# Optimization experiments

Measured on AMD Instinct MI355X. Metric: run time of the kernel, lower is better.

## Reference

```python
import math
import jax, jax.numpy as jnp
import numpy as np

B, NH, T, N, D = 4, 8, 2048, 256, 512
THETA = 2 ** 16
LN_EPS = 1e-5
RETRIEVAL_SCALE = 1.0
TWO_PI = 2.0 * math.pi


def _freqs(n):
    # get_freqs: 1/theta**(floor(i/2)*2 / n) / (2*pi)
    i = jnp.arange(n, dtype=jnp.float32)
    q = jnp.floor(i / 2.0) * 2.0
    return 1.0 / (THETA ** (q / n)) / TWO_PI


def _rope(phases, v):
    # phases: [1,1,T,N]; v: [B,nh,T,N]
    ph = (phases % 1.0) * TWO_PI
    pc, ps = jnp.cos(ph), jnp.sin(ph)
    ve, vo = v[..., ::2], v[..., 1::2]
    v_rot = jnp.stack((-vo, ve), axis=-1).reshape(v.shape)  # interleaved rotate
    return v * pc + v_rot * ps


def _l2norm(x):
    return x / jnp.maximum(jnp.linalg.norm(x, axis=-1, keepdims=True), 1e-12)


def setup_inputs() -> dict:
    key = jax.random.key(0)
    ks = jax.random.split(key, 8)
    return {
        "Q": jax.random.normal(ks[0], (B, NH, T, N), jnp.float32),
        "V": jax.random.normal(ks[1], (B, NH, T, D), jnp.float32),
        "x_raw": jax.random.normal(ks[2], (B, T, D), jnp.float32),
        "x_next": jax.random.normal(ks[3], (B, T, D), jnp.float32),
        "theta_Q_w": 0.02 * jax.random.normal(ks[4], (N, D), jnp.float32),
        "theta_K_w": 0.02 * jax.random.normal(ks[5], (N, D), jnp.float32),
        "beta_w": 0.02 * jax.random.normal(ks[6], (NH, D), jnp.float32),
        "memory_gate": jnp.full((1, NH, 1, 1), -2.0, jnp.float32),
        "M0": 0.02 * jax.random.normal(ks[7], (B, NH, N, D), jnp.float32),
    }


def _forward(Q, V, x_raw, x_next, theta_Q_w, theta_K_w, beta_w, memory_gate, M0):
    Bq, nh, Tq, Nq = Q.shape
    # ---- causal RoPE linear attention (K is Q; strictly lower-triangular, no softmax)
    freqs = _freqs(Nq)  # [N]
    phases = jnp.arange(Tq, dtype=jnp.float32)[None, None, :, None] * freqs[None, None, None, :]
    QR = _rope(phases, Q)
    scores = jnp.einsum('bhtn,bhsn->bhts', QR, QR)
    mask = jnp.tril(jnp.ones((Tq, Tq), bool), -1)  # diagonal=-1
    scores = jnp.where(mask, scores, 0.0)
    y_standard = scores @ V  # [B,nh,T,D]

    # ---- memory retrieval (position-invariant query)
    Qm = _l2norm(x_raw @ theta_Q_w.T)  # [B,T,N], shared across heads
    y_memory = jnp.einsum('btn,bhnd->bhtd', Qm, M0)
    mu = y_memory.mean(-1, keepdims=True)
    var = y_memory.var(-1, keepdims=True)  # biased, like torch LayerNorm
    y_memory = (y_memory - mu) * jax.lax.rsqrt(var + LN_EPS) * RETRIEVAL_SCALE

    # ---- delta-rule memory update (detached in the original)
    Km = _l2norm(jax.lax.stop_gradient(x_raw @ theta_K_w.T))         # [B,T,N]
    beta = jax.nn.sigmoid(jax.lax.stop_gradient(x_raw @ beta_w.T))   # [B,T,nh]
    Vm = jax.lax.stop_gradient(x_next)                               # [B,T,D]
    M_init = jax.lax.stop_gradient(M0)

    def step(M, inp):
        k, v, b = inp  # k:[B,N] shared across heads, v:[B,D], b:[B,nh]
        v_old = jnp.einsum('bn,bhnd->bhd', k, M)
        v_new = b[..., None] * v[:, None, :] + (1.0 - b[..., None]) * v_old
        M = M + jnp.einsum('bn,bhd->bhnd', k, v_new - v_old)
        return M, None

    M_new, _ = jax.lax.scan(
        step, M_init,
        (jnp.swapaxes(Km, 0, 1), jnp.swapaxes(Vm, 0, 1), jnp.swapaxes(beta, 0, 1)))

    gate = jax.nn.sigmoid(memory_gate)  # [1,nh,1,1]
    y = (1.0 - gate) * y_standard + gate * y_memory
    return y, M_new


def reference(Q, V, x_raw, x_next, theta_Q_w, theta_K_w, beta_w, memory_gate, M0):
    return _forward(Q, V, x_raw, x_next, theta_Q_w, theta_K_w, beta_w, memory_gate, M0)
```

## Files before the change

### kernel.cpp

```cpp
#include <hip/hip_runtime.h>
#include <hip/hip_bf16.h>
#include <math.h>

#define BBATCH 4
#define NHEAD  8
#define TSEQ   2048
#define NDIM   256
#define DDIM   512

typedef float f32x4 __attribute__((ext_vector_type(4)));
typedef short bf16x8 __attribute__((ext_vector_type(8)));

typedef __attribute__((address_space(3))) unsigned int lds_uint;
typedef __attribute__((address_space(1))) unsigned int g_uint;

__device__ __forceinline__ unsigned short f2bf(float f) {
  __hip_bfloat16 h = __float2bfloat16(f);
  return *reinterpret_cast<unsigned short*>(&h);
}
__device__ __forceinline__ float bf2f(unsigned short u) {
  __hip_bfloat16 h;
  *reinterpret_cast<unsigned short*>(&h) = u;
  return __bfloat162float(h);
}
__device__ __forceinline__ f32x4 mfma16(bf16x8 a, bf16x8 b, f32x4 c) {
  return __builtin_amdgcn_mfma_f32_16x16x32_bf16(a, b, c, 0, 0, 0);
}

#define KSW(t) (((((t) & 7) ^ (((t) >> 3) & 3))) << 4)

__global__ __launch_bounds__(256) void rope_kernel(const float* __restrict__ Q,
                                                   unsigned short* __restrict__ QR) {
  long idx = (long)blockIdx.x * 256 + threadIdx.x;
  int pair = (int)(idx & 127);
  long row = idx >> 7;
  int t = (int)(row & (TSEQ - 1));
  float2 q = reinterpret_cast<const float2*>(Q)[idx];
  float freq = exp2f(-(float)pair * 0.125f) * 0.15915494309189535f;
  float phase = (float)t * freq;
  float ph = (phase - floorf(phase)) * 6.283185307179586f;
  float s, c;
  sincosf(ph, &s, &c);
  float o0 = q.x * c - q.y * s;
  float o1 = q.y * c + q.x * s;
  unsigned int pk = (unsigned int)f2bf(o0) | ((unsigned int)f2bf(o1) << 16);
  reinterpret_cast<unsigned int*>(QR)[idx] = pk;
}

__global__ __launch_bounds__(256) void transpose_cast_kernel(
    const float* __restrict__ in, unsigned short* __restrict__ out, int R, int C) {
  __shared__ float tile[64][65];
  long mat = blockIdx.z;
  const float* src = in + mat * (long)R * C;
  unsigned short* dst = out + mat * (long)R * C;
  int c0 = blockIdx.x * 64, r0 = blockIdx.y * 64;
  int tr = threadIdx.x >> 4;
  int tc = (threadIdx.x & 15) * 4;
#pragma unroll
  for (int p = 0; p < 4; ++p) {
    int r = tr + p * 16;
    float4 v = *reinterpret_cast<const float4*>(&src[(long)(r0 + r) * C + c0 + tc]);
    tile[r][tc + 0] = v.x; tile[r][tc + 1] = v.y;
    tile[r][tc + 2] = v.z; tile[r][tc + 3] = v.w;
  }
  __syncthreads();
#pragma unroll
  for (int p = 0; p < 4; ++p) {
    int c = tr + p * 16;
    ushort4 o;
    o.x = f2bf(tile[tc + 0][c]);
    o.y = f2bf(tile[tc + 1][c]);
    o.z = f2bf(tile[tc + 2][c]);
    o.w = f2bf(tile[tc + 3][c]);
    *reinterpret_cast<ushort4*>(&dst[(long)(c0 + c) * R + r0 + tc]) = o;
  }
}

__global__ __launch_bounds__(512) void qkm_kernel(
    const float* __restrict__ x,
    const float* __restrict__ wq,
    const float* __restrict__ wk,
    unsigned short* __restrict__ Qm,
    float* __restrict__ Km,
    unsigned short* __restrict__ Kmb) {
  const bool isK = (blockIdx.y == 1);
  const float* w = isK ? wk : wq;
  int r0 = blockIdx.x * 64;
  int wave = threadIdx.x >> 6, lane = threadIdx.x & 63;
  int wm = wave >> 2, wn = wave & 3;
  int khi = lane >> 4, l16 = lane & 15;
  __shared__ unsigned short Ahi[64 * 32], Alo[64 * 32];
  __shared__ unsigned short Bhi[256 * 32], Blo[256 * 32];
  __shared__ float red[4][64];
  f32x4 acc[2][4] = {};
  for (int k0 = 0; k0 < 512; k0 += 32) {
    {
      int row = threadIdx.x >> 3;
      int kc = (threadIdx.x & 7) * 4;
      float4 v = *reinterpret_cast<const float4*>(&x[(long)(r0 + row) * 512 + k0 + kc]);
      float vv[4] = {v.x, v.y, v.z, v.w};
      unsigned int hx[2], lx[2];
      unsigned short h0 = f2bf(vv[0]), h1 = f2bf(vv[1]), h2 = f2bf(vv[2]), h3 = f2bf(vv[3]);
      hx[0] = (unsigned)h0 | ((unsigned)h1 << 16);
      hx[1] = (unsigned)h2 | ((unsigned)h3 << 16);
      lx[0] = (unsigned)f2bf(vv[0] - bf2f(h0)) | ((unsigned)f2bf(vv[1] - bf2f(h1)) << 16);
      lx[1] = (unsigned)f2bf(vv[2] - bf2f(h2)) | ((unsigned)f2bf(vv[3] - bf2f(h3)) << 16);
      int byt = row * 64 + ((kc * 2) ^ ((row & 3) << 4));
      *reinterpret_cast<uint2*>((char*)Ahi + byt) = make_uint2(hx[0], hx[1]);
      *reinterpret_cast<uint2*>((char*)Alo + byt) = make_uint2(lx[0], lx[1]);
    }
#pragma unroll
    for (int p = 0; p < 4; ++p) {
      int idx2 = threadIdx.x + p * 512;
      int row = idx2 >> 3;
      int kc = (idx2 & 7) * 4;
      float4 v = *reinterpret_cast<const float4*>(&w[(long)row * 512 + k0 + kc]);
      float vv[4] = {v.x, v.y, v.z, v.w};
      unsigned short h0 = f2bf(vv[0]), h1 = f2bf(vv[1]), h2 = f2bf(vv[2]), h3 = f2bf(vv[3]);
      unsigned int hx0 = (unsigned)h0 | ((unsigned)h1 << 16);
      unsigned int hx1 = (unsigned)h2 | ((unsigned)h3 << 16);
      unsigned int lx0 = (unsigned)f2bf(vv[0] - bf2f(h0)) | ((unsigned)f2bf(vv[1] - bf2f(h1)) << 16);
      unsigned int lx1 = (unsigned)f2bf(vv[2] - bf2f(h2)) | ((unsigned)f2bf(vv[3] - bf2f(h3)) << 16);
      int byt = row * 64 + ((kc * 2) ^ ((row & 3) << 4));
      *reinterpret_cast<uint2*>((char*)Bhi + byt) = make_uint2(hx0, hx1);
      *reinterpret_cast<uint2*>((char*)Blo + byt) = make_uint2(lx0, lx1);
    }
    __syncthreads();
    bf16x8 ah[2], al[2], bh[4], bl[4];
#pragma unroll
    for (int mi = 0; mi < 2; ++mi) {
      int row = wm * 32 + mi * 16 + l16;
      int byt = row * 64 + ((khi * 16) ^ ((row & 3) << 4));
      ah[mi] = *reinterpret_cast<const bf16x8*>((const char*)Ahi + byt);
      al[mi] = *reinterpret_cast<const bf16x8*>((const char*)Alo + byt);
    }
#pragma unroll
    for (int ni = 0; ni < 4; ++ni) {
      int row = wn * 64 + ni * 16 + l16;
      int byt = row * 64 + ((khi * 16) ^ ((row & 3) << 4));
      bh[ni] = *reinterpret_cast<const bf16x8*>((const char*)Bhi + byt);
      bl[ni] = *reinterpret_cast<const bf16x8*>((const char*)Blo + byt);
    }
#pragma unroll
    for (int mi = 0; mi < 2; ++mi)
#pragma unroll
      for (int ni = 0; ni < 4; ++ni) {
        acc[mi][ni] = mfma16(ah[mi], bh[ni], acc[mi][ni]);
        acc[mi][ni] = mfma16(ah[mi], bl[ni], acc[mi][ni]);
        acc[mi][ni] = mfma16(al[mi], bh[ni], acc[mi][ni]);
      }
    __syncthreads();
  }
  float part[2][4];
#pragma unroll
  for (int mi = 0; mi < 2; ++mi)
#pragma unroll
    for (int r = 0; r < 4; ++r) {
      float s = 0.f;
#pragma unroll
      for (int ni = 0; ni < 4; ++ni) s += acc[mi][ni][r] * acc[mi][ni][r];
      part[mi][r] = s;
    }
#pragma unroll
  for (int off = 1; off < 16; off <<= 1)
#pragma unroll
    for (int mi = 0; mi < 2; ++mi)
#pragma unroll
      for (int r = 0; r < 4; ++r) part[mi][r] += __shfl_xor(part[mi][r], off);
  if (l16 == 0) {
#pragma unroll
    for (int mi = 0; mi < 2; ++mi)
#pragma unroll
      for (int r = 0; r < 4; ++r)
        red[wn][wm * 32 + mi * 16 + khi * 4 + r] = part[mi][r];
  }
  __syncthreads();
#pragma unroll
  for (int mi = 0; mi < 2; ++mi)
#pragma unroll
    for (int r = 0; r < 4; ++r) {
      int row = wm * 32 + mi * 16 + khi * 4 + r;
      float ss = red[0][row] + red[1][row] + red[2][row] + red[3][row];
      float scale = 1.f / fmaxf(sqrtf(ss), 1e-12f);
#pragma unroll
      for (int ni = 0; ni < 4; ++ni) {
        int col = wn * 64 + ni * 16 + l16;
        float val = acc[mi][ni][r] * scale;
        if (isK) {
          Km[(long)(r0 + row) * 256 + col] = val;
          Kmb[(long)(r0 + row) * 256 + col] = f2bf(val);
        } else {
          Qm[(long)(r0 + row) * 256 + col] = f2bf(val);
        }
      }
    }
}

__global__ __launch_bounds__(64) void beta_kernel(const float* __restrict__ x,
                                                  const float* __restrict__ bw,
                                                  float* __restrict__ beta) {
  long row = blockIdx.x;
  int lane = threadIdx.x;
  const float* xr = x + row * 512;
  float xv[8];
#pragma unroll
  for (int j = 0; j < 8; ++j) xv[j] = xr[lane + j * 64];
#pragma unroll
  for (int hh = 0; hh < 8; ++hh) {
    const float* wr = bw + hh * 512;
    float p = 0.f;
#pragma unroll
    for (int j = 0; j < 8; ++j) p += xv[j] * wr[lane + j * 64];
#pragma unroll
    for (int off = 32; off > 0; off >>= 1) p += __shfl_down(p, off);
    if (lane == 0) beta[row * 8 + hh] = 1.f / (1.f + expf(-p));
  }
}

__global__ __launch_bounds__(256) void wprep_kernel(
    const float* __restrict__ Km, const float* __restrict__ beta,
    unsigned short* __restrict__ Whi, unsigned short* __restrict__ Wlo) {
  __shared__ unsigned short Khi[64 * 256];
  __shared__ unsigned short Klo[64 * 256];
  __shared__ float Bm[64 * 64];
  __shared__ float bv[64];
  int blk = blockIdx.x, ch = blk & 31, bh = blk >> 5;
  int b = bh >> 3, h = bh & 7;
  int t0 = ch * 64;
  int tid = threadIdx.x, wave = tid >> 6, lane = tid & 63;
  int khi = lane >> 4, l16 = lane & 15;
  {
    int t = tid >> 2, n0 = (tid & 3) * 64;
    const float* kp = Km + ((long)(b * TSEQ) + t0 + t) * 256 + n0;
    char* ph = (char*)Khi + t * 512;
    char* pl = (char*)Klo + t * 512;
#pragma unroll
    for (int i = 0; i < 64; i += 8) {
      float4 v0 = *(const float4*)(kp + i);
      float4 v1 = *(const float4*)(kp + i + 4);
      float vv[8] = {v0.x, v0.y, v0.z, v0.w, v1.x, v1.y, v1.z, v1.w};
      unsigned int hw[4], lw[4];
#pragma unroll
      for (int q = 0; q < 4; ++q) {
        unsigned short h0 = f2bf(vv[2 * q]), h1 = f2bf(vv[2 * q + 1]);
        hw[q] = (unsigned)h0 | ((unsigned)h1 << 16);
        lw[q] = (unsigned)f2bf(vv[2 * q] - bf2f(h0)) |
                ((unsigned)f2bf(vv[2 * q + 1] - bf2f(h1)) << 16);
      }
      int off = ((n0 + i) * 2) ^ ((t & 7) << 4);
      *(uint4*)(ph + off) = make_uint4(hw[0], hw[1], hw[2], hw[3]);
      *(uint4*)(pl + off) = make_uint4(lw[0], lw[1], lw[2], lw[3]);
    }
  }
  if (tid < 64) bv[tid] = beta[((long)(b * TSEQ) + t0 + tid) * 8 + h];
  __syncthreads();
  f32x4 sacc[4] = {};
#pragma unroll
  for (int ks = 0; ks < 8; ++ks) {
    int arow = wave * 16 + l16;
    int koff = (ks * 32 + khi * 8) * 2;
    bf16x8 ah = *(const bf16x8*)((const char*)Khi + arow * 512 + (koff ^ ((arow & 7) << 4)));
    bf16x8 al = *(const bf16x8*)((const char*)Klo + arow * 512 + (koff ^ ((arow & 7) << 4)));
    bf16x8 bhf[4], blf[4];
#pragma unroll
    for (int si = 0; si < 4; ++si) {
      int brow = si * 16 + l16;
      bhf[si] = *(const bf16x8*)((const char*)Khi + brow * 512 + (koff ^ ((brow & 7) << 4)));
      blf[si] = *(const bf16x8*)((const char*)Klo + brow * 512 + (koff ^ ((brow & 7) << 4)));
    }
#pragma unroll
    for (int si = 0; si < 4; ++si) sacc[si] = mfma16(ah, bhf[si], sacc[si]);
#pragma unroll
    for (int si = 0; si < 4; ++si) sacc[si] = mfma16(ah, blf[si], sacc[si]);
#pragma unroll
    for (int si = 0; si < 4; ++si) sacc[si] = mfma16(al, bhf[si], sacc[si]);
  }
#pragma unroll
  for (int si = 0; si < 4; ++si)
#pragma unroll
    for (int r = 0; r < 4; ++r) {
      int t = wave * 16 + khi * 4 + r, s = si * 16 + l16;
      Bm[t * 64 + s] = (s < t) ? bv[t] * sacc[si][r] : 0.f;
    }
  __syncthreads();
  if (wave == 0) {
    float x[64];
#pragma unroll
    for (int i = 0; i < 64; ++i) x[i] = 0.f;
    long base = (long)blk * 4096;
    const f32x4* BmV = (const f32x4*)Bm;
    float bl = bv[lane];
#pragma unroll
    for (int t = 0; t < 64; ++t) {
      float p0 = 0.f, p1 = 0.f, p2 = 0.f, p3 = 0.f;
#pragma unroll
      for (int rq = 0; rq < 16; ++rq) {
        f32x4 b4 = BmV[t * 16 + rq];
        p0 = fmaf(b4.x, x[rq * 4 + 0], p0);
        p1 = fmaf(b4.y, x[rq * 4 + 1], p1);
        p2 = fmaf(b4.z, x[rq * 4 + 2], p2);
        p3 = fmaf(b4.w, x[rq * 4 + 3], p3);
      }
      float xv = ((lane == t) ? 1.f : 0.f) - ((p0 + p1) + (p2 + p3));
      x[t] = xv;
      float wv = xv * bl;
      unsigned short hi = f2bf(wv);
      Whi[base + t * 64 + lane] = hi;
      Wlo[base + t * 64 + lane] = f2bf(wv - bf2f(hi));
    }
  }
}

__global__ __launch_bounds__(512) void cscan_kernel(
    const unsigned short* __restrict__ Kb,
    const unsigned short* __restrict__ KbT,
    const float* __restrict__ xn,
    const float* __restrict__ M0,
    const unsigned short* __restrict__ Whi,
    const unsigned short* __restrict__ Wlo,
    float* __restrict__ Mout) {
  __shared__ unsigned short Mthi[64 * 256];
  __shared__ unsigned short Mtlo[64 * 256];
  __shared__ unsigned short Kr[64 * 256];
  __shared__ unsigned short Pool[16384];
  __shared__ unsigned short RU0[64 * 64];
  __shared__ unsigned short RU1[64 * 64];
  unsigned short* Wh = Pool;
  unsigned short* Wl = Pool + 4096;
  unsigned short* Krt = Pool;
  int bh = blockIdx.x, dsl = blockIdx.y;
  int b = bh >> 3;
  int d0 = dsl * 64;
  int tid = threadIdx.x, wave = tid >> 6, lane = tid & 63;
  int khi = lane >> 4, l16 = lane & 15;
  int tq = wave & 3, dh = wave >> 2;
  const char* KbBase = (const char*)(Kb + (long)b * TSEQ * 256);

  f32x4 macc[2][4];
  const float* M0p = M0 + (long)bh * 256 * 512;
#pragma unroll
  for (int ni = 0; ni < 2; ++ni)
#pragma unroll
    for (int di = 0; di < 4; ++di)
#pragma unroll
      for (int r = 0; r < 4; ++r) {
        int n = wave * 32 + ni * 16 + khi * 4 + r;
        macc[ni][di][r] = M0p[(long)n * 512 + d0 + di * 16 + l16];
      }
#pragma unroll
  for (int ni = 0; ni < 2; ++ni)
#pragma unroll
    for (int di = 0; di < 4; ++di) {
      int n = wave * 32 + ni * 16 + khi * 4;
      int d = di * 16 + l16;
      unsigned short hq[4], lq[4];
#pragma unroll
      for (int r = 0; r < 4; ++r) {
        float v = macc[ni][di][r];
        hq[r] = f2bf(v); lq[r] = f2bf(v - bf2f(hq[r]));
      }
      int off = d * 512 + (((n * 2) ^ ((d & 7) << 4)));
      *(uint2*)((char*)Mthi + off) =
          make_uint2((unsigned)hq[0] | ((unsigned)hq[1] << 16),
                     (unsigned)hq[2] | ((unsigned)hq[3] << 16));
      *(uint2*)((char*)Mtlo + off) =
          make_uint2((unsigned)lq[0] | ((unsigned)lq[1] << 16),
                     (unsigned)lq[2] | ((unsigned)lq[3] << 16));
    }
#pragma unroll
  for (int q = 0; q < 4; ++q) {
    int lin = tid * 16 + q * 8192;
    int t = lin >> 9;
    int c = (lin & 511) ^ KSW(t);
    __builtin_amdgcn_global_load_lds((const g_uint*)(KbBase + (long)t * 512 + c),
                                     (lds_uint*)((char*)Kr + lin), 16, 0, 0);
  }
  __syncthreads();

  for (int ch = 0; ch < 32; ++ch) {
    int tc0 = ch * 64;
    {
      const char* whb = (const char*)(Whi + ((long)bh * 32 + ch) * 4096);
      const char* wlb = (const char*)(Wlo + ((long)bh * 32 + ch) * 4096);
      int lin = tid * 16;
      int t = lin >> 7, c = lin & 127;
      int sb = t * 128 + (c ^ ((t & 7) << 4));
      __builtin_amdgcn_global_load_lds((const g_uint*)(whb + sb),
                                       (lds_uint*)((char*)Wh + lin), 16, 0, 0);
      __builtin_amdgcn_global_load_lds((const g_uint*)(wlb + sb),
                                       (lds_uint*)((char*)Wl + lin), 16, 0, 0);
    }
    float vreg[2][4];
    {
      const float* vp = xn + ((long)b * TSEQ + tc0) * 512 + d0;
#pragma unroll
      for (int di = 0; di < 2; ++di)
#pragma unroll
        for (int r = 0; r < 4; ++r) {
          int t = tq * 16 + khi * 4 + r;
          vreg[di][r] = vp[(long)t * 512 + (dh * 2 + di) * 16 + l16];
        }
    }
    __syncthreads();

    f32x4 aacc[2] = {};
#pragma unroll
    for (int ks = 0; ks < 8; ++ks) {
      int arow = tq * 16 + l16;
      int koff = (ks * 32 + khi * 8) * 2;
      bf16x8 af = *(const bf16x8*)((const char*)Kr + arow * 512 + (koff ^ KSW(arow)));
      bf16x8 mh[2], ml[2];
#pragma unroll
      for (int di = 0; di < 2; ++di) {
        int drow = (dh * 2 + di) * 16 + l16;
        mh[di] = *(const bf16x8*)((const char*)Mthi + drow * 512 + (koff ^ ((drow & 7) << 4)));
        ml[di] = *(const bf16x8*)((const char*)Mtlo + drow * 512 + (koff ^ ((drow & 7) << 4)));
      }
#pragma unroll
      for (int di = 0; di < 2; ++di) aacc[di] = mfma16(af, mh[di], aacc[di]);
#pragma unroll
      for (int di = 0; di < 2; ++di) aacc[di] = mfma16(af, ml[di], aacc[di]);
    }
#pragma unroll
    for (int di = 0; di < 2; ++di) {
      int t = tq * 16 + khi * 4;
      int d = (dh * 2 + di) * 16 + l16;
      unsigned short rq[4];
#pragma unroll
      for (int r = 0; r < 4; ++r) rq[r] = f2bf(vreg[di][r] - aacc[di][r]);
      int off = d * 128 + (((t * 2) ^ ((d & 7) << 4)));
      *(uint2*)((char*)RU0 + off) =
          make_uint2((unsigned)rq[0] | ((unsigned)rq[1] << 16),
                     (unsigned)rq[2] | ((unsigned)rq[3] << 16));
    }
    __syncthreads();

    if (ch + 1 < 32) {
      const char* kb2 = KbBase + (long)(tc0 + 64) * 512;
#pragma unroll
      for (int q = 0; q < 4; ++q) {
        int lin = tid * 16 + q * 8192;
        int t = lin >> 9;
        int c = (lin & 511) ^ KSW(t);
        __builtin_amdgcn_global_load_lds((const g_uint*)(kb2 + (long)t * 512 + c),
                                         (lds_uint*)((char*)Kr + lin), 16, 0, 0);
      }
    }

    f32x4 uacc[2] = {};
#pragma unroll
    for (int ks = 0; ks < 2; ++ks) {
      int arow = tq * 16 + l16;
      int soff = (ks * 32 + khi * 8) * 2;
      bf16x8 wh_ = *(const bf16x8*)((const char*)Wh + arow * 128 + (soff ^ ((arow & 7) << 4)));
      bf16x8 wl_ = *(const bf16x8*)((const char*)Wl + arow * 128 + (soff ^ ((arow & 7) << 4)));
      bf16x8 rf[2];
#pragma unroll
      for (int di = 0; di < 2; ++di) {
        int drow = (dh * 2 + di) * 16 + l16;
        rf[di] = *(const bf16x8*)((const char*)RU0 + drow * 128 + (soff ^ ((drow & 7) << 4)));
      }
#pragma unroll
      for (int di = 0; di < 2; ++di) uacc[di] = mfma16(wh_, rf[di], uacc[di]);
#pragma unroll
      for (int di = 0; di < 2; ++di) uacc[di] = mfma16(wl_, rf[di], uacc[di]);
    }
    __syncthreads();

    {
#pragma unroll
      for (int q = 0; q < 4; ++q) {
        int lin = tid * 16 + q * 8192;
        int n = lin >> 7, c = lin & 127;
        long sb = ((long)(b * 256 + n)) * 4096 + (long)tc0 * 2 + (c ^ ((n & 7) << 4));
        __builtin_amdgcn_global_load_lds((const g_uint*)((const char*)KbT + sb),
                                         (lds_uint*)((char*)Krt + lin), 16, 0, 0);
      }
    }
#pragma unroll
    for (int di = 0; di < 2; ++di) {
      int t = tq * 16 + khi * 4;
      int d = (dh * 2 + di) * 16 + l16;
      unsigned short hq[4], lq[4];
#pragma unroll
      for (int r = 0; r < 4; ++r) {
        float u = uacc[di][r];
        hq[r] = f2bf(u); lq[r] = f2bf(u - bf2f(hq[r]));
      }
      int off = d * 128 + (((t * 2) ^ ((d & 7) << 4)));
      *(uint2*)((char*)RU0 + off) =
          make_uint2((unsigned)hq[0] | ((unsigned)hq[1] << 16),
                     (unsigned)hq[2] | ((unsigned)hq[3] << 16));
      *(uint2*)((char*)RU1 + off) =
          make_uint2((unsigned)lq[0] | ((unsigned)lq[1] << 16),
                     (unsigned)lq[2] | ((unsigned)lq[3] << 16));
    }
    __syncthreads();

#pragma unroll
    for (int ks = 0; ks < 2; ++ks) {
      int toff = (ks * 32 + khi * 8) * 2;
      bf16x8 ka[2];
#pragma unroll
      for (int ni = 0; ni < 2; ++ni) {
        int n = wave * 32 + ni * 16 + l16;
        ka[ni] = *(const bf16x8*)((const char*)Krt + n * 128 + (toff ^ ((n & 7) << 4)));
      }
      bf16x8 uh[4], ul[4];
#pragma unroll
      for (int di = 0; di < 4; ++di) {
        int drow = di * 16 + l16;
        uh[di] = *(const bf16x8*)((const char*)RU0 + drow * 128 + (toff ^ ((drow & 7) << 4)));
        ul[di] = *(const bf16x8*)((const char*)RU1 + drow * 128 + (toff ^ ((drow & 7) << 4)));
      }
#pragma unroll
      for (int ni = 0; ni < 2; ++ni)
#pragma unroll
        for (int di = 0; di < 4; ++di)
          macc[ni][di] = mfma16(ka[ni], uh[di], macc[ni][di]);
#pragma unroll
      for (int ni = 0; ni < 2; ++ni)
#pragma unroll
        for (int di = 0; di < 4; ++di)
          macc[ni][di] = mfma16(ka[ni], ul[di], macc[ni][di]);
    }
#pragma unroll
    for (int ni = 0; ni < 2; ++ni)
#pragma unroll
      for (int di = 0; di < 4; ++di) {
        int n = wave * 32 + ni * 16 + khi * 4;
        int d = di * 16 + l16;
        unsigned short hq[4], lq[4];
#pragma unroll
        for (int r = 0; r < 4; ++r) {
          float v = macc[ni][di][r];
          hq[r] = f2bf(v); lq[r] = f2bf(v - bf2f(hq[r]));
        }
        int off = d * 512 + (((n * 2) ^ ((d & 7) << 4)));
        *(uint2*)((char*)Mthi + off) =
            make_uint2((unsigned)hq[0] | ((unsigned)hq[1] << 16),
                       (unsigned)hq[2] | ((unsigned)hq[3] << 16));
        *(uint2*)((char*)Mtlo + off) =
            make_uint2((unsigned)lq[0] | ((unsigned)lq[1] << 16),
                       (unsigned)lq[2] | ((unsigned)lq[3] << 16));
      }
    __syncthreads();
  }

  float* Mo = Mout + (long)bh * 256 * 512;
#pragma unroll
  for (int ni = 0; ni < 2; ++ni)
#pragma unroll
    for (int di = 0; di < 4; ++di)
#pragma unroll
      for (int r = 0; r < 4; ++r) {
        int n = wave * 32 + ni * 16 + khi * 4 + r;
        Mo[(long)n * 512 + d0 + di * 16 + l16] = macc[ni][di][r];
      }
}

__global__ __launch_bounds__(512) void attn_kernel(
    const unsigned short* __restrict__ QR,
    const unsigned short* __restrict__ Vt,
    float* __restrict__ Y) {
  int bh = blockIdx.x;
  int bp = blockIdx.y;
  int wave = threadIdx.x >> 6, lane = threadIdx.x & 63;
  int wr = wave >> 2, wc = wave & 3;
  int khi = lane >> 4, l16 = lane & 15;
  __shared__ unsigned short K_lds[2][64 * 256];
  __shared__ unsigned short S_lds[128 * 64];
  const unsigned short* QRb = QR + (long)bh * TSEQ * 256;
  const unsigned short* Vtb = Vt + (long)bh * 512 * TSEQ;
  float* yb = Y + (long)bh * TSEQ * 512;
  int lin_base = wave * 4096 + lane * 16;

#pragma unroll 1
  for (int half = 0; half < 2; ++half) {
    int bt = half ? bp : (15 - bp);
    int t0 = bt * 128;
    int nst = 2 * bt + 2;

    bf16x8 qa[8];
    {
      int trow = t0 + wave * 16 + l16;
      const unsigned short* qp = QRb + (long)trow * 256 + khi * 8;
#pragma unroll
      for (int ks = 0; ks < 8; ++ks) qa[ks] = *(const bf16x8*)(qp + ks * 32);
    }
    f32x4 acc[4][8] = {};

#pragma unroll
    for (int q = 0; q < 4; ++q) {
      int linear = lin_base + q * 1024;
      int row = linear >> 9;
      int nc2 = (linear & 511) ^ ((row & 7) << 4);
      __builtin_amdgcn_global_load_lds(
          (const g_uint*)((const char*)QRb + (long)row * 512 + nc2),
          (lds_uint*)((char*)K_lds[0] + (wave * 4 + q) * 1024), 16, 0, 0);
    }
    __syncthreads();

    for (int st = 0; st < nst; ++st) {
      int s0 = st * 64;
      const char* Kcur = (const char*)K_lds[st & 1];

      if (st + 1 < nst) {
        long srow_base = (long)(s0 + 64) * 512;
        char* Knext = (char*)K_lds[(st + 1) & 1];
#pragma unroll
        for (int q = 0; q < 4; ++q) {
          int linear = lin_base + q * 1024;
          int row = linear >> 9;
          int nc2 = (linear & 511) ^ ((row & 7) << 4);
          __builtin_amdgcn_global_load_lds(
              (const g_uint*)((const char*)QRb + srow_base + (long)row * 512 + nc2),
              (lds_uint*)(Knext + (wave * 4 + q) * 1024), 16, 0, 0);
        }
      }

      f32x4 sacc[4] = {};
#pragma unroll
      for (int ks = 0; ks < 8; ++ks) {
#pragma unroll
        for (int fc = 0; fc < 4; ++fc) {
          int srow = fc * 16 + l16;
          bf16x8 kf = *(const bf16x8*)(
              Kcur + srow * 512 + ((ks * 64 + khi * 16) ^ ((srow & 7) << 4)));
          sacc[fc] = mfma16(qa[ks], kf, sacc[fc]);
        }
      }
#pragma unroll
      for (int fc = 0; fc < 4; ++fc)
#pragma unroll
        for (int r = 0; r < 4; ++r) {
          int srow = wave * 16 + khi * 4 + r;
          int scol = fc * 16 + l16;
          float v = ((s0 + scol) < (t0 + srow)) ? sacc[fc][r] : 0.f;
          *(unsigned short*)(
              (char*)S_lds + srow * 128 + ((scol * 2) ^ ((srow & 7) << 4))) = f2bf(v);
        }
      __syncthreads();

#pragma unroll
      for (int k2 = 0; k2 < 2; ++k2) {
        bf16x8 af[4];
#pragma unroll
        for (int mi = 0; mi < 4; ++mi) {
          int row = wr * 64 + mi * 16 + l16;
          af[mi] = *(const bf16x8*)(
              (const char*)S_lds + row * 128 + ((k2 * 64 + khi * 16) ^ ((row & 7) << 4)));
        }
#pragma unroll
        for (int nh = 0; nh < 2; ++nh) {
          bf16x8 bfv[4];
#pragma unroll
          for (int nj = 0; nj < 4; ++nj) {
            int d = wc * 128 + (nh * 4 + nj) * 16 + l16;
            bfv[nj] = *(const bf16x8*)(Vtb + (long)d * TSEQ + s0 + k2 * 32 + khi * 8);
          }
#pragma unroll
          for (int mi = 0; mi < 4; ++mi)
#pragma unroll
            for (int nj = 0; nj < 4; ++nj)
              acc[mi][nh * 4 + nj] = mfma16(af[mi], bfv[nj], acc[mi][nh * 4 + nj]);
        }
      }
      __syncthreads();
    }

#pragma unroll
    for (int mi = 0; mi < 4; ++mi)
#pragma unroll
      for (int ni = 0; ni < 8; ++ni)
#pragma unroll
        for (int r = 0; r < 4; ++r) {
          int trow = t0 + wr * 64 + mi * 16 + khi * 4 + r;
          int d = wc * 128 + ni * 16 + l16;
          yb[(long)trow * 512 + d] = acc[mi][ni][r];
        }
  }
}

__global__ __launch_bounds__(512) void combine_kernel(
    const unsigned short* __restrict__ Qm,
    const unsigned short* __restrict__ M0t,
    const float* __restrict__ mg,
    float* __restrict__ Y) {
  int t0 = blockIdx.x * 64;
  int bh = blockIdx.y;
  int b = bh >> 3, h = bh & 7;
  int wv = threadIdx.x >> 6, lane = threadIdx.x & 63;
  int khi = lane >> 4, l16 = lane & 15;
  __shared__ unsigned short A_lds[64 * 256];
  __shared__ float red_s[8][64], red_q[8][64];
  __shared__ float mu_s[64], inv_s[64];
  {
    const unsigned short* src = Qm + ((long)b * TSEQ + t0) * 256;
#pragma unroll
    for (int p = 0; p < 4; ++p) {
      int row = (threadIdx.x >> 5) + p * 16;
      int nc = (threadIdx.x & 31) * 8;
      bf16x8 v = *reinterpret_cast<const bf16x8*>(src + (long)row * 256 + nc);
      *reinterpret_cast<bf16x8*>((char*)A_lds + row * 512 + ((nc * 2) ^ ((row & 7) << 4))) = v;
    }
  }
  __syncthreads();
  f32x4 acc[4][4] = {};
  const unsigned short* Bp = M0t + (long)bh * 512 * 256;
#pragma unroll
  for (int ks = 0; ks < 8; ++ks) {
    bf16x8 a[4], bfr[4];
#pragma unroll
    for (int mi = 0; mi < 4; ++mi) {
      int row = mi * 16 + l16;
      a[mi] = *reinterpret_cast<const bf16x8*>(
          (const char*)A_lds + row * 512 + ((ks * 64 + khi * 16) ^ ((row & 7) << 4)));
    }
#pragma unroll
    for (int ni = 0; ni < 4; ++ni) {
      int d = wv * 64 + ni * 16 + l16;
      bfr[ni] = *reinterpret_cast<const bf16x8*>(Bp + (long)d * 256 + ks * 32 + khi * 8);
    }
#pragma unroll
    for (int mi = 0; mi < 4; ++mi)
#pragma unroll
      for (int ni = 0; ni < 4; ++ni)
        acc[mi][ni] = mfma16(a[mi], bfr[ni], acc[mi][ni]);
  }
  float ps[4][4], pq[4][4];
#pragma unroll
  for (int mi = 0; mi < 4; ++mi)
#pragma unroll
    for (int r = 0; r < 4; ++r) {
      float s = 0.f, q = 0.f;
#pragma unroll
      for (int ni = 0; ni < 4; ++ni) {
        float v = acc[mi][ni][r];
        s += v; q += v * v;
      }
      ps[mi][r] = s; pq[mi][r] = q;
    }
#pragma unroll
  for (int off = 1; off < 16; off <<= 1)
#pragma unroll
    for (int mi = 0; mi < 4; ++mi)
#pragma unroll
      for (int r = 0; r < 4; ++r) {
        ps[mi][r] += __shfl_xor(ps[mi][r], off);
        pq[mi][r] += __shfl_xor(pq[mi][r], off);
      }
  if (l16 == 0) {
#pragma unroll
    for (int mi = 0; mi < 4; ++mi)
#pragma unroll
      for (int r = 0; r < 4; ++r) {
        int row = mi * 16 + khi * 4 + r;
        red_s[wv][row] = ps[mi][r];
        red_q[wv][row] = pq[mi][r];
      }
  }
  __syncthreads();
  if (threadIdx.x < 64) {
    float s = 0.f, q = 0.f;
#pragma unroll
    for (int w2 = 0; w2 < 8; ++w2) { s += red_s[w2][threadIdx.x]; q += red_q[w2][threadIdx.x]; }
    float mu = s / 512.f;
    float var = q / 512.f - mu * mu;
    mu_s[threadIdx.x] = mu;
    inv_s[threadIdx.x] = rsqrtf(var + 1e-5f);
  }
  __syncthreads();
  float gate = 1.f / (1.f + expf(-mg[h]));
  float omg = 1.f - gate;
  float* yb = Y + ((long)bh * TSEQ + t0) * 512;
#pragma unroll
  for (int mi = 0; mi < 4; ++mi)
#pragma unroll
    for (int r = 0; r < 4; ++r) {
      int row = mi * 16 + khi * 4 + r;
      float mu = mu_s[row], inv = inv_s[row];
#pragma unroll
      for (int ni = 0; ni < 4; ++ni) {
        int d = wv * 64 + ni * 16 + l16;
        long off = (long)row * 512 + d;
        float ymv = (acc[mi][ni][r] - mu) * inv;
        yb[off] = omg * yb[off] + gate * ymv;
      }
    }
}

extern "C" void kernel_launch(void* const* d_in, const int* in_sizes, int n_in,
                              void* d_out, int out_size, void* d_ws, size_t ws_size,
                              hipStream_t stream) {
  const float* Q      = (const float*)d_in[0];
  const float* V      = (const float*)d_in[1];
  const float* x_raw  = (const float*)d_in[2];
  const float* x_next = (const float*)d_in[3];
  const float* wq     = (const float*)d_in[4];
  const float* wk     = (const float*)d_in[5];
  const float* bw     = (const float*)d_in[6];
  const float* mg     = (const float*)d_in[7];
  const float* M0     = (const float*)d_in[8];
  float* y = (float*)d_out;
  float* Mout = y + (long)32 * 2048 * 512;

  char* ws = (char*)d_ws;
  unsigned short* QR  = (unsigned short*)(ws);
  unsigned short* Vt  = (unsigned short*)(ws + 33554432);
  unsigned short* M0t = (unsigned short*)(ws + 100663296);
  unsigned short* Qm  = (unsigned short*)(ws + 109051904);
  float*  Km          = (float*)(ws + 113246208);
  float*  beta        = (float*)(ws + 121634816);
  unsigned short* Whi = (unsigned short*)(ws + 33554432);
  unsigned short* Wlo = (unsigned short*)(ws + 41943040);
  unsigned short* Kmb = (unsigned short*)(ws + 50331648);
  unsigned short* KmT = (unsigned short*)(ws + 54525952);

  qkm_kernel<<<dim3(128, 2), dim3(512), 0, stream>>>(x_raw, wq, wk, Qm, Km, Kmb);
  transpose_cast_kernel<<<dim3(4, 32, 4), dim3(256), 0, stream>>>(Km, KmT, 2048, 256);
  beta_kernel<<<dim3(8192), dim3(64), 0, stream>>>(x_raw, bw, beta);
  wprep_kernel<<<dim3(1024), dim3(256), 0, stream>>>(Km, beta, Whi, Wlo);
  cscan_kernel<<<dim3(32, 8), dim3(512), 0, stream>>>(Kmb, KmT, x_next, M0, Whi, Wlo, Mout);
  rope_kernel<<<dim3(32768), dim3(256), 0, stream>>>(Q, QR);
  transpose_cast_kernel<<<dim3(8, 32, 32), dim3(256), 0, stream>>>(V, Vt, 2048, 512);
  transpose_cast_kernel<<<dim3(8, 4, 32), dim3(256), 0, stream>>>(M0, M0t, 256, 512);
  attn_kernel<<<dim3(32, 8), dim3(512), 0, stream>>>(QR, Vt, y);
  combine_kernel<<<dim3(32, 32), dim3(512), 0, stream>>>(Qm, M0t, mg, y);
}
```

Measured before the change: 705.9 us.

## Read K, K^T and W operands directly from global to shrink LDS in chunked scan

Removes the Kr and Pool LDS staging buffers in the chunked delta-rule scan kernel. MFMA operands K, K^T and the WY factors now come straight from global memory (expected to hit L2) instead of async global-to-LDS copies. One barrier is dropped and launch bounds ask for two blocks per CU, aiming for higher occupancy. The cost is global-load latency on the serial critical path of each chunk and the loss of the prefetch overlap the async LDS loads gave.

```diff
diff --git a/kernel.cpp b/kernel.cpp
--- a/kernel.cpp
+++ b/kernel.cpp
@@ -311,7 +311,7 @@
   }
 }
 
-__global__ __launch_bounds__(512) void cscan_kernel(
+__global__ __launch_bounds__(512, 2) void cscan_kernel(
     const unsigned short* __restrict__ Kb,
     const unsigned short* __restrict__ KbT,
     const float* __restrict__ xn,
@@ -321,20 +321,16 @@
     float* __restrict__ Mout) {
   __shared__ unsigned short Mthi[64 * 256];
   __shared__ unsigned short Mtlo[64 * 256];
-  __shared__ unsigned short Kr[64 * 256];
-  __shared__ unsigned short Pool[16384];
   __shared__ unsigned short RU0[64 * 64];
   __shared__ unsigned short RU1[64 * 64];
-  unsigned short* Wh = Pool;
-  unsigned short* Wl = Pool + 4096;
-  unsigned short* Krt = Pool;
   int bh = blockIdx.x, dsl = blockIdx.y;
   int b = bh >> 3;
   int d0 = dsl * 64;
   int tid = threadIdx.x, wave = tid >> 6, lane = tid & 63;
   int khi = lane >> 4, l16 = lane & 15;
   int tq = wave & 3, dh = wave >> 2;
-  const char* KbBase = (const char*)(Kb + (long)b * TSEQ * 256);
+  const unsigned short* Kg  = Kb  + (long)b * TSEQ * 256;
+  const unsigned short* KTg = KbT + (long)b * 256 * TSEQ;
 
   f32x4 macc[2][4];
   const float* M0p = M0 + (long)bh * 256 * 512;
@@ -367,29 +363,10 @@
           make_uint2((unsigned)lq[0] | ((unsigned)lq[1] << 16),
                      (unsigned)lq[2] | ((unsigned)lq[3] << 16));
     }
-#pragma unroll
-  for (int q = 0; q < 4; ++q) {
-    int lin = tid * 16 + q * 8192;
-    int t = lin >> 9;
-    int c = (lin & 511) ^ KSW(t);
-    __builtin_amdgcn_global_load_lds((const g_uint*)(KbBase + (long)t * 512 + c),
-                                     (lds_uint*)((char*)Kr + lin), 16, 0, 0);
-  }
   __syncthreads();
 
   for (int ch = 0; ch < 32; ++ch) {
     int tc0 = ch * 64;
-    {
-      const char* whb = (const char*)(Whi + ((long)bh * 32 + ch) * 4096);
-      const char* wlb = (const char*)(Wlo + ((long)bh * 32 + ch) * 4096);
-      int lin = tid * 16;
-      int t = lin >> 7, c = lin & 127;
-      int sb = t * 128 + (c ^ ((t & 7) << 4));
-      __builtin_amdgcn_global_load_lds((const g_uint*)(whb + sb),
-                                       (lds_uint*)((char*)Wh + lin), 16, 0, 0);
-      __builtin_amdgcn_global_load_lds((const g_uint*)(wlb + sb),
-                                       (lds_uint*)((char*)Wl + lin), 16, 0, 0);
-    }
     float vreg[2][4];
     {
       const float* vp = xn + ((long)b * TSEQ + tc0) * 512 + d0;
@@ -401,14 +378,13 @@
           vreg[di][r] = vp[(long)t * 512 + (dh * 2 + di) * 16 + l16];
         }
     }
-    __syncthreads();
 
     f32x4 aacc[2] = {};
 #pragma unroll
     for (int ks = 0; ks < 8; ++ks) {
       int arow = tq * 16 + l16;
       int koff = (ks * 32 + khi * 8) * 2;
-      bf16x8 af = *(const bf16x8*)((const char*)Kr + arow * 512 + (koff ^ KSW(arow)));
+      bf16x8 af = *(const bf16x8*)(Kg + (long)(tc0 + arow) * 256 + ks * 32 + khi * 8);
       bf16x8 mh[2], ml[2];
 #pragma unroll
       for (int di = 0; di < 2; ++di) {
@@ -435,48 +411,30 @@
     }
     __syncthreads();
 
-    if (ch + 1 < 32) {
-      const char* kb2 = KbBase + (long)(tc0 + 64) * 512;
-#pragma unroll
-      for (int q = 0; q < 4; ++q) {
-        int lin = tid * 16 + q * 8192;
-        int t = lin >> 9;
-        int c = (lin & 511) ^ KSW(t);
-        __builtin_amdgcn_global_load_lds((const g_uint*)(kb2 + (long)t * 512 + c),
-                                         (lds_uint*)((char*)Kr + lin), 16, 0, 0);
-      }
-    }
-
     f32x4 uacc[2] = {};
-#pragma unroll
-    for (int ks = 0; ks < 2; ++ks) {
-      int arow = tq * 16 + l16;
-      int soff = (ks * 32 + khi * 8) * 2;
-      bf16x8 wh_ = *(const bf16x8*)((const char*)Wh + arow * 128 + (soff ^ ((arow & 7) << 4)));
-      bf16x8 wl_ = *(const bf16x8*)((const char*)Wl + arow * 128 + (soff ^ ((arow & 7) << 4)));
-      bf16x8 rf[2];
-#pragma unroll
-      for (int di = 0; di < 2; ++di) {
-        int drow = (dh * 2 + di) * 16 + l16;
-        rf[di] = *(const bf16x8*)((const char*)RU0 + drow * 128 + (soff ^ ((drow & 7) << 4)));
-      }
-#pragma unroll
-      for (int di = 0; di < 2; ++di) uacc[di] = mfma16(wh_, rf[di], uacc[di]);
-#pragma unroll
-      for (int di = 0; di < 2; ++di) uacc[di] = mfma16(wl_, rf[di], uacc[di]);
+    {
+      const unsigned short* Wg  = Whi + ((long)bh * 32 + ch) * 4096;
+      const unsigned short* Wlg = Wlo + ((long)bh * 32 + ch) * 4096;
+#pragma unroll
+      for (int ks = 0; ks < 2; ++ks) {
+        int arow = tq * 16 + l16;
+        int soff = (ks * 32 + khi * 8) * 2;
+        bf16x8 wh_ = *(const bf16x8*)(Wg  + arow * 64 + ks * 32 + khi * 8);
+        bf16x8 wl_ = *(const bf16x8*)(Wlg + arow * 64 + ks * 32 + khi * 8);
+        bf16x8 rf[2];
+#pragma unroll
+        for (int di = 0; di < 2; ++di) {
+          int drow = (dh * 2 + di) * 16 + l16;
+          rf[di] = *(const bf16x8*)((const char*)RU0 + drow * 128 + (soff ^ ((drow & 7) << 4)));
+        }
+#pragma unroll
+        for (int di = 0; di < 2; ++di) uacc[di] = mfma16(wh_, rf[di], uacc[di]);
+#pragma unroll
+        for (int di = 0; di < 2; ++di) uacc[di] = mfma16(wl_, rf[di], uacc[di]);
+      }
     }
     __syncthreads();
 
-    {
-#pragma unroll
-      for (int q = 0; q < 4; ++q) {
-        int lin = tid * 16 + q * 8192;
-        int n = lin >> 7, c = lin & 127;
-        long sb = ((long)(b * 256 + n)) * 4096 + (long)tc0 * 2 + (c ^ ((n & 7) << 4));
-        __builtin_amdgcn_global_load_lds((const g_uint*)((const char*)KbT + sb),
-                                         (lds_uint*)((char*)Krt + lin), 16, 0, 0);
-      }
-    }
 #pragma unroll
     for (int di = 0; di < 2; ++di) {
       int t = tq * 16 + khi * 4;
@@ -504,7 +462,7 @@
 #pragma unroll
       for (int ni = 0; ni < 2; ++ni) {
         int n = wave * 32 + ni * 16 + l16;
-        ka[ni] = *(const bf16x8*)((const char*)Krt + n * 128 + (toff ^ ((n & 7) << 4)));
+        ka[ni] = *(const bf16x8*)(KTg + (long)n * TSEQ + tc0 + ks * 32 + khi * 8);
       }
       bf16x8 uh[4], ul[4];
 #pragma unroll
```

Measured after the change: 748.3 us. +6.0%, slower.

## Split chunked scan over 32-wide D slices and read K directly from global

Applied to the files above, without the earlier changes.

The delta-rule chunked scan now runs 512 blocks with 32-column D slices instead of 256 blocks with 64 columns. Each block holds half the memory state in LDS and registers, and launch bounds allow two blocks per CU. The LDS staging buffer for K rows is dropped in favour of direct global loads into MFMA fragments, which shrinks LDS use and removes one prefetch and one barrier per chunk. The cost is that the per-chunk W and K-transpose loads are repeated by twice as many blocks, and the K fragment reads become uncached-layout global loads on the critical path.

```diff
diff --git a/kernel.cpp b/kernel.cpp
--- a/kernel.cpp
+++ b/kernel.cpp
@@ -311,7 +311,7 @@
   }
 }
 
-__global__ __launch_bounds__(512) void cscan_kernel(
+__global__ __launch_bounds__(512, 2) void cscan_kernel(
     const unsigned short* __restrict__ Kb,
     const unsigned short* __restrict__ KbT,
     const float* __restrict__ xn,
@@ -319,29 +319,28 @@
     const unsigned short* __restrict__ Whi,
     const unsigned short* __restrict__ Wlo,
     float* __restrict__ Mout) {
-  __shared__ unsigned short Mthi[64 * 256];
-  __shared__ unsigned short Mtlo[64 * 256];
-  __shared__ unsigned short Kr[64 * 256];
+  __shared__ unsigned short Mthi[32 * 256];
+  __shared__ unsigned short Mtlo[32 * 256];
   __shared__ unsigned short Pool[16384];
-  __shared__ unsigned short RU0[64 * 64];
-  __shared__ unsigned short RU1[64 * 64];
+  __shared__ unsigned short RU0[32 * 64];
+  __shared__ unsigned short RU1[32 * 64];
   unsigned short* Wh = Pool;
   unsigned short* Wl = Pool + 4096;
   unsigned short* Krt = Pool;
   int bh = blockIdx.x, dsl = blockIdx.y;
   int b = bh >> 3;
-  int d0 = dsl * 64;
+  int d0 = dsl * 32;
   int tid = threadIdx.x, wave = tid >> 6, lane = tid & 63;
   int khi = lane >> 4, l16 = lane & 15;
   int tq = wave & 3, dh = wave >> 2;
-  const char* KbBase = (const char*)(Kb + (long)b * TSEQ * 256);
-
-  f32x4 macc[2][4];
+  const unsigned short* Kg = Kb + (long)b * TSEQ * 256;
+
+  f32x4 macc[2][2];
   const float* M0p = M0 + (long)bh * 256 * 512;
 #pragma unroll
   for (int ni = 0; ni < 2; ++ni)
 #pragma unroll
-    for (int di = 0; di < 4; ++di)
+    for (int di = 0; di < 2; ++di)
 #pragma unroll
       for (int r = 0; r < 4; ++r) {
         int n = wave * 32 + ni * 16 + khi * 4 + r;
@@ -350,7 +349,7 @@
 #pragma unroll
   for (int ni = 0; ni < 2; ++ni)
 #pragma unroll
-    for (int di = 0; di < 4; ++di) {
+    for (int di = 0; di < 2; ++di) {
       int n = wave * 32 + ni * 16 + khi * 4;
       int d = di * 16 + l16;
       unsigned short hq[4], lq[4];
@@ -367,14 +366,6 @@
           make_uint2((unsigned)lq[0] | ((unsigned)lq[1] << 16),
                      (unsigned)lq[2] | ((unsigned)lq[3] << 16));
     }
-#pragma unroll
-  for (int q = 0; q < 4; ++q) {
-    int lin = tid * 16 + q * 8192;
-    int t = lin >> 9;
-    int c = (lin & 511) ^ KSW(t);
-    __builtin_amdgcn_global_load_lds((const g_uint*)(KbBase + (long)t * 512 + c),
-                                     (lds_uint*)((char*)Kr + lin), 16, 0, 0);
-  }
   __syncthreads();
 
   for (int ch = 0; ch < 32; ++ch) {
@@ -390,44 +381,34 @@
       __builtin_amdgcn_global_load_lds((const g_uint*)(wlb + sb),
                                        (lds_uint*)((char*)Wl + lin), 16, 0, 0);
     }
-    float vreg[2][4];
+    float vreg[4];
     {
       const float* vp = xn + ((long)b * TSEQ + tc0) * 512 + d0;
 #pragma unroll
-      for (int di = 0; di < 2; ++di)
-#pragma unroll
-        for (int r = 0; r < 4; ++r) {
-          int t = tq * 16 + khi * 4 + r;
-          vreg[di][r] = vp[(long)t * 512 + (dh * 2 + di) * 16 + l16];
-        }
-    }
-    __syncthreads();
-
-    f32x4 aacc[2] = {};
+      for (int r = 0; r < 4; ++r) {
+        int t = tq * 16 + khi * 4 + r;
+        vreg[r] = vp[(long)t * 512 + dh * 16 + l16];
+      }
+    }
+
+    f32x4 aacc = {};
 #pragma unroll
     for (int ks = 0; ks < 8; ++ks) {
       int arow = tq * 16 + l16;
       int koff = (ks * 32 + khi * 8) * 2;
-      bf16x8 af = *(const bf16x8*)((const char*)Kr + arow * 512 + (koff ^ KSW(arow)));
-      bf16x8 mh[2], ml[2];
-#pragma unroll
-      for (int di = 0; di < 2; ++di) {
-        int drow = (dh * 2 + di) * 16 + l16;
-        mh[di] = *(const bf16x8*)((const char*)Mthi + drow * 512 + (koff ^ ((drow & 7) << 4)));
-        ml[di] = *(const bf16x8*)((const char*)Mtlo + drow * 512 + (koff ^ ((drow & 7) << 4)));
-      }
-#pragma unroll
-      for (int di = 0; di < 2; ++di) aacc[di] = mfma16(af, mh[di], aacc[di]);
-#pragma unroll
-      for (int di = 0; di < 2; ++di) aacc[di] = mfma16(af, ml[di], aacc[di]);
-    }
-#pragma unroll
-    for (int di = 0; di < 2; ++di) {
+      bf16x8 af = *(const bf16x8*)(Kg + (long)(tc0 + arow) * 256 + ks * 32 + khi * 8);
+      int drow = dh * 16 + l16;
+      bf16x8 mh = *(const bf16x8*)((const char*)Mthi + drow * 512 + (koff ^ ((drow & 7) << 4)));
+      bf16x8 ml = *(const bf16x8*)((const char*)Mtlo + drow * 512 + (koff ^ ((drow & 7) << 4)));
+      aacc = mfma16(af, mh, aacc);
+      aacc = mfma16(af, ml, aacc);
+    }
+    {
       int t = tq * 16 + khi * 4;
-      int d = (dh * 2 + di) * 16 + l16;
+      int d = dh * 16 + l16;
       unsigned short rq[4];
 #pragma unroll
-      for (int r = 0; r < 4; ++r) rq[r] = f2bf(vreg[di][r] - aacc[di][r]);
+      for (int r = 0; r < 4; ++r) rq[r] = f2bf(vreg[r] - aacc[r]);
       int off = d * 128 + (((t * 2) ^ ((d & 7) << 4)));
       *(uint2*)((char*)RU0 + off) =
           make_uint2((unsigned)rq[0] | ((unsigned)rq[1] << 16),
@@ -435,35 +416,17 @@
     }
     __syncthreads();
 
-    if (ch + 1 < 32) {
-      const char* kb2 = KbBase + (long)(tc0 + 64) * 512;
-#pragma unroll
-      for (int q = 0; q < 4; ++q) {
-        int lin = tid * 16 + q * 8192;
-        int t = lin >> 9;
-        int c = (lin & 511) ^ KSW(t);
-        __builtin_amdgcn_global_load_lds((const g_uint*)(kb2 + (long)t * 512 + c),
-                                         (lds_uint*)((char*)Kr + lin), 16, 0, 0);
-      }
-    }
-
-    f32x4 uacc[2] = {};
+    f32x4 uacc = {};
 #pragma unroll
     for (int ks = 0; ks < 2; ++ks) {
       int arow = tq * 16 + l16;
       int soff = (ks * 32 + khi * 8) * 2;
       bf16x8 wh_ = *(const bf16x8*)((const char*)Wh + arow * 128 + (soff ^ ((arow & 7) << 4)));
       bf16x8 wl_ = *(const bf16x8*)((const char*)Wl + arow * 128 + (soff ^ ((arow & 7) << 4)));
-      bf16x8 rf[2];
-#pragma unroll
-      for (int di = 0; di < 2; ++di) {
-        int drow = (dh * 2 + di) * 16 + l16;
-        rf[di] = *(const bf16x8*)((const char*)RU0 + drow * 128 + (soff ^ ((drow & 7) << 4)));
-      }
-#pragma unroll
-      for (int di = 0; di < 2; ++di) uacc[di] = mfma16(wh_, rf[di], uacc[di]);
-#pragma unroll
-      for (int di = 0; di < 2; ++di) uacc[di] = mfma16(wl_, rf[di], uacc[di]);
+      int drow = dh * 16 + l16;
+      bf16x8 rf = *(const bf16x8*)((const char*)RU0 + drow * 128 + (soff ^ ((drow & 7) << 4)));
+      uacc = mfma16(wh_, rf, uacc);
+      uacc = mfma16(wl_, rf, uacc);
     }
     __syncthreads();
 
@@ -477,14 +440,13 @@
                                          (lds_uint*)((char*)Krt + lin), 16, 0, 0);
       }
     }
-#pragma unroll
-    for (int di = 0; di < 2; ++di) {
+    {
       int t = tq * 16 + khi * 4;
-      int d = (dh * 2 + di) * 16 + l16;
+      int d = dh * 16 + l16;
       unsigned short hq[4], lq[4];
 #pragma unroll
       for (int r = 0; r < 4; ++r) {
-        float u = uacc[di][r];
+        float u = uacc[r];
         hq[r] = f2bf(u); lq[r] = f2bf(u - bf2f(hq[r]));
       }
       int off = d * 128 + (((t * 2) ^ ((d & 7) << 4)));
@@ -506,9 +468,9 @@
         int n = wave * 32 + ni * 16 + l16;
         ka[ni] = *(const bf16x8*)((const char*)Krt + n * 128 + (toff ^ ((n & 7) << 4)));
       }
-      bf16x8 uh[4], ul[4];
-#pragma unroll
-      for (int di = 0; di < 4; ++di) {
+      bf16x8 uh[2], ul[2];
+#pragma unroll
+      for (int di = 0; di < 2; ++di) {
         int drow = di * 16 + l16;
         uh[di] = *(const bf16x8*)((const char*)RU0 + drow * 128 + (toff ^ ((drow & 7) << 4)));
         ul[di] = *(const bf16x8*)((const char*)RU1 + drow * 128 + (toff ^ ((drow & 7) << 4)));
@@ -516,18 +478,18 @@
 #pragma unroll
       for (int ni = 0; ni < 2; ++ni)
 #pragma unroll
-        for (int di = 0; di < 4; ++di)
+        for (int di = 0; di < 2; ++di)
           macc[ni][di] = mfma16(ka[ni], uh[di], macc[ni][di]);
 #pragma unroll
       for (int ni = 0; ni < 2; ++ni)
 #pragma unroll
-        for (int di = 0; di < 4; ++di)
+        for (int di = 0; di < 2; ++di)
           macc[ni][di] = mfma16(ka[ni], ul[di], macc[ni][di]);
     }
 #pragma unroll
     for (int ni = 0; ni < 2; ++ni)
 #pragma unroll
-      for (int di = 0; di < 4; ++di) {
+      for (int di = 0; di < 2; ++di) {
         int n = wave * 32 + ni * 16 + khi * 4;
         int d = di * 16 + l16;
         unsigned short hq[4], lq[4];
@@ -551,7 +513,7 @@
 #pragma unroll
   for (int ni = 0; ni < 2; ++ni)
 #pragma unroll
-    for (int di = 0; di < 4; ++di)
+    for (int di = 0; di < 2; ++di)
 #pragma unroll
       for (int r = 0; r < 4; ++r) {
         int n = wave * 32 + ni * 16 + khi * 4 + r;
@@ -821,7 +783,7 @@
   transpose_cast_kernel<<<dim3(4, 32, 4), dim3(256), 0, stream>>>(Km, KmT, 2048, 256);
   beta_kernel<<<dim3(8192), dim3(64), 0, stream>>>(x_raw, bw, beta);
   wprep_kernel<<<dim3(1024), dim3(256), 0, stream>>>(Km, beta, Whi, Wlo);
-  cscan_kernel<<<dim3(32, 8), dim3(512), 0, stream>>>(Kmb, KmT, x_next, M0, Whi, Wlo, Mout);
+  cscan_kernel<<<dim3(32, 16), dim3(512), 0, stream>>>(Kmb, KmT, x_next, M0, Whi, Wlo, Mout);
   rope_kernel<<<dim3(32768), dim3(256), 0, stream>>>(Q, QR);
   transpose_cast_kernel<<<dim3(8, 32, 32), dim3(256), 0, stream>>>(V, Vt, 2048, 512);
   transpose_cast_kernel<<<dim3(8, 4, 32), dim3(256), 0, stream>>>(M0, M0t, 256, 512);
```

Measured after the change: 750.1 us. 1.06x slower.
